# Kernel tuning notes

Measured on AMD Instinct MI355X. Metric: run time of the kernel, lower is better.

Reference implementation:

```python
import jax, jax.numpy as jnp
import numpy as np

# SparseSphereConv (graph_level=6 -> V=40962, kernel_size=9, stride=1, select_index=None)
# Pipeline: neighbor gather -> data-dependent nonzero row selection ->
# per-vertex KxK interpolation matmul -> 1xK conv (linear over C_in,K) -> scatter back.
# With stride=1 / select_index=None the static selection is the identity, so the
# dynamic nonzero selection is equivalent to computing all rows and zeroing the
# rows whose gathered features are entirely zero (selected rows are scattered back,
# unselected rows stay 0 in sparse_reset's zero-initialized output).

BS, C_IN, C_OUT, V, K = 4, 32, 32, 40962, 9

def setup_inputs() -> dict:
    key = jax.random.key(0)
    k1, k2, k3, k4, k5 = jax.random.split(key, 5)
    x = jax.random.normal(k1, (BS, C_IN, V), dtype=jnp.float32)
    index = jax.random.randint(k2, (V, K), 0, V, dtype=jnp.int32)          # neighbor ids per vertex
    itp_mat = jax.random.uniform(k3, (V, K, K), dtype=jnp.float32)         # per-vertex interpolation
    conv_w = jax.random.normal(k4, (C_OUT, C_IN, K), dtype=jnp.float32) * 0.05  # Conv2d(C_in,C_out,(1,K)) weight
    conv_b = jax.random.normal(k5, (C_OUT,), dtype=jnp.float32) * 0.05
    return {"x": x, "index": index, "itp_mat": itp_mat, "conv_w": conv_w, "conv_b": conv_b}

def reference(x, index, itp_mat, conv_w, conv_b):
    # x: [bs, C, V] -> permute(2,0,1) -> gather neighbors -> [V, K, bs, C]
    g = jnp.transpose(x, (2, 0, 1))[index]
    g = jnp.transpose(g, (3, 2, 0, 1))                      # [C, bs, V, K]  (== reshape of [C, bs*V, K])
    # sparse_prepare: keep rows whose min or max over (C, K) is nonzero (detached in torch)
    gd = jax.lax.stop_gradient(g)
    rmin = gd.min(axis=(0, 3))                              # [bs, V]
    rmax = gd.max(axis=(0, 3))                              # [bs, V]
    mask = (rmin != 0) | (rmax != 0)                        # [bs, V]
    # Interploate: [C, S, 1, K] @ [S, K, K] per row -> batched small matmul
    interp = jnp.einsum('cbvk,vkj->cbvj', g, itp_mat)       # [C, bs, V, K]
    # Conv2d with kernel (1, K): contraction over (C_in, K) + bias
    out = jnp.einsum('cbvk,ock->bov', interp, conv_w) + conv_b[None, :, None]  # [bs, C_out, V]
    # sparse_reset: rows not selected stay zero
    return out * mask[:, None, :].astype(out.dtype)
```

## Files before the change

kernel.cpp:

```cpp
#include <hip/hip_runtime.h>
#include <hip/hip_bf16.h>

#define NV 40962
#define NK 9
#define CIN 32
#define COUT 32
#define NBS 4
#define VT 256
#define TP 260
#define NT 2561
#define NV81 (NV * 81)
#define NV9  (NV * 9)

typedef __attribute__((ext_vector_type(8))) short bf16x8;
typedef __attribute__((ext_vector_type(4))) float f32x4;
typedef __attribute__((ext_vector_type(2))) float f32x2;

#define PKFMA_L(A, G, R) asm("v_pk_fma_f32 %0, %1, %2, %0 op_sel:[0,0,0] op_sel_hi:[0,1,1]" : "+v"(A) : "v"(G), "v"(R))
#define PKFMA_H(A, G, R) asm("v_pk_fma_f32 %0, %1, %2, %0 op_sel:[1,0,0] op_sel_hi:[1,1,1]" : "+v"(A) : "v"(G), "v"(R))
#define PKMUL_L(A, G, R) asm("v_pk_mul_f32 %0, %1, %2 op_sel:[0,0] op_sel_hi:[0,1]" : "=v"(A) : "v"(G), "v"(R))
#define PKMUL_H(A, G, R) asm("v_pk_mul_f32 %0, %1, %2 op_sel:[1,0] op_sel_hi:[1,1]" : "=v"(A) : "v"(G), "v"(R))

#define ACC(cc, j) ((j) == 8 ? acc8[cc] : (((j) & 1) ? acc2[cc][(j) >> 1].y \
                                                     : acc2[cc][(j) >> 1].x))

__device__ __forceinline__ unsigned pkbf(float a, float b) {
    union { __hip_bfloat162 h2; unsigned u; } cv;
    cv.h2 = __float22bfloat162_rn(make_float2(a, b));
    return cv.u;
}

__global__ void __launch_bounds__(256) transpose_x_bf16(
    const float* __restrict__ x, unsigned* __restrict__ xtw)
{
    __shared__ unsigned T[16 * TP];
    const int b  = blockIdx.x & 3;
    const int v0 = (blockIdx.x >> 2) * VT;
    const int t  = threadIdx.x;
    const int w  = t >> 6;
    const int L  = t & 63;
    const bool full = (v0 + VT <= NV);

    #pragma unroll
    for (int i = 0; i < 4; ++i) {
        const int q = w + 4 * i;
        const float* rowA = x + (size_t)(b * 32 + 2 * q) * NV;
        const float* rowB = rowA + NV;
        #pragma unroll
        for (int h = 0; h < 2; ++h) {
            const int vl = 128 * h + 2 * L;
            float2 a, c;
            if (full) {
                a = *(const float2*)(rowA + v0 + vl);
                c = *(const float2*)(rowB + v0 + vl);
            } else {
                const int v = v0 + vl;
                a.x = (v     < NV) ? rowA[v]     : 0.0f;
                a.y = (v + 1 < NV) ? rowA[v + 1] : 0.0f;
                c.x = (v     < NV) ? rowB[v]     : 0.0f;
                c.y = (v + 1 < NV) ? rowB[v + 1] : 0.0f;
            }
            uint2 d;
            d.x = pkbf(a.x, c.x);
            d.y = pkbf(a.y, c.y);
            *(uint2*)&T[q * TP + vl] = d;
        }
    }
    __syncthreads();

    #pragma unroll
    for (int i = 0; i < 4; ++i) {
        const int vl = i * 64 + w * 16 + (L >> 2);
        const int u4 = L & 3;
        const int v  = v0 + vl;
        if (v < NV) {
            uint4 d;
            d.x = T[(4 * u4 + 0) * TP + vl];
            d.y = T[(4 * u4 + 1) * TP + vl];
            d.z = T[(4 * u4 + 2) * TP + vl];
            d.w = T[(4 * u4 + 3) * TP + vl];
            *(uint4*)&xtw[(size_t)v * 64 + b * 16 + 4 * u4] = d;
        }
    }
}

__global__ void __launch_bounds__(256) convert_w_bf16(
    const float* __restrict__ w, unsigned short* __restrict__ wbf)
{
    const int i = blockIdx.x * 256 + threadIdx.x;
    if (i < COUT * CIN * NK) {
        const int o = i / 288;
        const int r = i - o * 288;
        const int c = r / 9;
        const int j = r - c * 9;
        unsigned u = __float_as_uint(w[i]);
        wbf[o * 288 + j * 32 + c] =
            (unsigned short)((u + 0x7FFFu + ((u >> 16) & 1u)) >> 16);
    }
}

__global__ void __launch_bounds__(256) sparse_conv_mfma(
    const unsigned short* __restrict__ xt, const int* __restrict__ index,
    const float* __restrict__ itp, const unsigned short* __restrict__ wbf,
    const float* __restrict__ bias, float* __restrict__ out)
{
    __shared__ unsigned short Wlds[9 * 32 * 32];
    __shared__ float itp_s[16 * 108];
    __shared__ int   idx_s[144];

    const int t    = threadIdx.x;
    const int b    = t >> 6;
    const int lane = t & 63;
    const int vloc = lane & 15;
    const int quad = lane >> 4;
    const int tile = blockIdx.x;

    float bs0[4], bs1[4];
    #pragma unroll
    for (int r = 0; r < 4; ++r) {
        bs0[r] = bias[quad * 4 + r];
        bs1[r] = bias[quad * 4 + 16 + r];
    }

    #pragma unroll
    for (int r = 0; r < 5; ++r) {
        const int n = t + r * 256;
        if (n < 1152) {
            const int j  = n >> 7;
            const int o  = (n >> 2) & 31;
            const int cq = n & 3;
            ((uint4*)Wlds)[n] = ((const uint4*)wbf)[o * 36 + j * 4 + cq];
        }
    }
    if (t < 144) {
        const size_t bix = (size_t)tile * 144 + t;
        idx_s[t] = (bix < (size_t)NV9) ? index[bix] : 0;
    }
    {
        float itpv[6];
        const size_t base = (size_t)tile * 1296;
        #pragma unroll
        for (int i = 0; i < 6; ++i) {
            const int o = i * 256 + t;
            itpv[i] = (o < 1296 && base + o < (size_t)NV81) ? itp[base + o]
                                                            : 0.0f;
        }
        #pragma unroll
        for (int i = 0; i < 6; ++i) {
            const int o = i * 256 + t;
            if (o < 1296) {
                const int vl = o / 81;
                const int r2 = o - vl * 81;
                const int kk = r2 / 9;
                const int jj = r2 - kk * 9;
                itp_s[vl * 108 + kk * 12 + jj] = itpv[i];
            }
        }
    }
    __syncthreads();

    int nbr[NK];
    #pragma unroll
    for (int n = 0; n < NK; ++n) nbr[n] = idx_s[vloc * 9 + n];

    const unsigned short* gbase = xt + b * 32 + quad * 8;
    uint2 g0[NK], g1[NK];
    #pragma unroll
    for (int n = 0; n < NK; ++n)
        g0[n] = *(const uint2*)(gbase + (size_t)nbr[n] * 128);
    #pragma unroll
    for (int n = 0; n < NK; ++n)
        g1[n] = *(const uint2*)(gbase + (size_t)nbr[n] * 128 + 4);

    unsigned frag[9][4];
    unsigned nzbits = 0;
    const float* ib = &itp_s[vloc * 108];

    #pragma unroll
    for (int h = 0; h < 2; ++h) {
        f32x2 acc2[4][4];
        float acc8[4];
        #pragma unroll
        for (int n = 0; n < NK; ++n) {
            const uint2 gk = h ? g1[n] : g0[n];
            nzbits |= (gk.x | gk.y) & 0x7FFF7FFFu;
            f32x2 gp01, gp23;
            gp01.x = __uint_as_float(gk.x << 16);
            gp01.y = __uint_as_float(gk.x & 0xFFFF0000u);
            gp23.x = __uint_as_float(gk.y << 16);
            gp23.y = __uint_as_float(gk.y & 0xFFFF0000u);
            const float* ir = ib + n * 12;
            const f32x4 ra = *(const f32x4*)ir;
            const f32x4 rb = *(const f32x4*)(ir + 4);
            const float r8 = ir[8];
            f32x2 rp[4];
            rp[0] = __builtin_shufflevector(ra, ra, 0, 1);
            rp[1] = __builtin_shufflevector(ra, ra, 2, 3);
            rp[2] = __builtin_shufflevector(rb, rb, 0, 1);
            rp[3] = __builtin_shufflevector(rb, rb, 2, 3);
            if (n == 0) {
                #pragma unroll
                for (int jp = 0; jp < 4; ++jp) {
                    PKMUL_L(acc2[0][jp], gp01, rp[jp]);
                    PKMUL_H(acc2[1][jp], gp01, rp[jp]);
                    PKMUL_L(acc2[2][jp], gp23, rp[jp]);
                    PKMUL_H(acc2[3][jp], gp23, rp[jp]);
                }
                acc8[0] = gp01.x * r8; acc8[1] = gp01.y * r8;
                acc8[2] = gp23.x * r8; acc8[3] = gp23.y * r8;
            } else {
                #pragma unroll
                for (int jp = 0; jp < 4; ++jp) {
                    PKFMA_L(acc2[0][jp], gp01, rp[jp]);
                    PKFMA_H(acc2[1][jp], gp01, rp[jp]);
                    PKFMA_L(acc2[2][jp], gp23, rp[jp]);
                    PKFMA_H(acc2[3][jp], gp23, rp[jp]);
                }
                acc8[0] += gp01.x * r8; acc8[1] += gp01.y * r8;
                acc8[2] += gp23.x * r8; acc8[3] += gp23.y * r8;
            }
        }
        #pragma unroll
        for (int ks = 0; ks < 9; ++ks) {
            frag[ks][2 * h]     = pkbf(ACC(0, ks), ACC(1, ks));
            frag[ks][2 * h + 1] = pkbf(ACC(2, ks), ACC(3, ks));
        }
    }

    unsigned nzw = nzbits;
    nzw |= __shfl_xor(nzw, 16);
    nzw |= __shfl_xor(nzw, 32);

    f32x4 c0 = {0.f, 0.f, 0.f, 0.f};
    f32x4 c1 = {0.f, 0.f, 0.f, 0.f};
    #pragma unroll
    for (int ks = 0; ks < 9; ++ks) {
        union { uint4 u; bf16x8 v; } bfr;
        bfr.u.x = frag[ks][0]; bfr.u.y = frag[ks][1];
        bfr.u.z = frag[ks][2]; bfr.u.w = frag[ks][3];
        const bf16x8 wa0 =
            *(const bf16x8*)&Wlds[(ks * 32 + vloc) * 32 + quad * 8];
        const bf16x8 wa1 =
            *(const bf16x8*)&Wlds[(ks * 32 + vloc + 16) * 32 + quad * 8];
        c0 = __builtin_amdgcn_mfma_f32_16x16x32_bf16(wa0, bfr.v, c0, 0, 0, 0);
        c1 = __builtin_amdgcn_mfma_f32_16x16x32_bf16(wa1, bfr.v, c1, 0, 0, 0);
    }

    const int vv = tile * 16 + vloc;
    if (vv < NV) {
        const float m = nzw ? 1.0f : 0.0f;
        float* ob = out + (size_t)b * (COUT * NV) + vv;
        #pragma unroll
        for (int r = 0; r < 4; ++r) {
            ob[(size_t)(quad * 4 + r) * NV]      = (c0[r] + bs0[r]) * m;
            ob[(size_t)(quad * 4 + 16 + r) * NV] = (c1[r] + bs1[r]) * m;
        }
    }
}

extern "C" void kernel_launch(void* const* d_in, const int* in_sizes, int n_in,
                              void* d_out, int out_size, void* d_ws, size_t ws_size,
                              hipStream_t stream)
{
    const float* x     = (const float*)d_in[0];
    const int*   index = (const int*)  d_in[1];
    const float* itp   = (const float*)d_in[2];
    const float* w     = (const float*)d_in[3];
    const float* bias  = (const float*)d_in[4];
    float*       out   = (float*)d_out;

    unsigned short* xt  = (unsigned short*)d_ws;
    unsigned short* wbf = (unsigned short*)((char*)d_ws + (size_t)NV * 256);

    hipLaunchKernelGGL(convert_w_bf16, dim3((COUT * CIN * NK + 255) / 256),
                       dim3(256), 0, stream, w, wbf);
    const int vtiles = (NV + VT - 1) / VT;
    hipLaunchKernelGGL(transpose_x_bf16, dim3(vtiles * NBS), dim3(256), 0,
                       stream, x, (unsigned*)xt);
    hipLaunchKernelGGL(sparse_conv_mfma, dim3(NT), dim3(256), 0,
                       stream, xt, index, itp, wbf, bias, out);
}
```

Before: 128.3 us.

## Remap lanes to batch-by-vertex and interleave bf16 layout for 16-byte gathers

The transposed bf16 buffer is re-laid out so that, for each vertex, the four batches of one 8-channel group sit next to each other. The conv kernel's lane mapping changes so each wave covers 4 vertices by 4 batches instead of 16 vertices of one batch. Each lane now fetches a neighbor's features with one 16-byte load instead of two 8-byte loads, and the lanes serving one vertex together read its full 256-byte row. The aim is fewer, better-coalesced gather transactions. The trade-off is that output stores now cover only 4 consecutive vertices per row segment, which weakens store coalescing.

```diff
diff --git a/kernel.cpp b/kernel.cpp
--- a/kernel.cpp
+++ b/kernel.cpp
@@ -79,7 +79,7 @@
             d.y = T[(4 * u4 + 1) * TP + vl];
             d.z = T[(4 * u4 + 2) * TP + vl];
             d.w = T[(4 * u4 + 3) * TP + vl];
-            *(uint4*)&xtw[(size_t)v * 64 + b * 16 + 4 * u4] = d;
+            *(uint4*)&xtw[(size_t)v * 64 + u4 * 16 + b * 4] = d;
         }
     }
 }
@@ -109,17 +109,20 @@
     __shared__ int   idx_s[144];
 
     const int t    = threadIdx.x;
-    const int b    = t >> 6;
+    const int w    = t >> 6;
     const int lane = t & 63;
-    const int vloc = lane & 15;
-    const int quad = lane >> 4;
+    const int arow = lane & 15;
+    const int coct = lane >> 4;
+    const int b    = (lane >> 2) & 3;
+    const int vv   = lane & 3;
+    const int vl   = w * 4 + vv;
     const int tile = blockIdx.x;
 
     float bs0[4], bs1[4];
     #pragma unroll
     for (int r = 0; r < 4; ++r) {
-        bs0[r] = bias[quad * 4 + r];
-        bs1[r] = bias[quad * 4 + 16 + r];
+        bs0[r] = bias[coct * 4 + r];
+        bs1[r] = bias[coct * 4 + 16 + r];
     }
 
     #pragma unroll
@@ -149,11 +152,11 @@
         for (int i = 0; i < 6; ++i) {
             const int o = i * 256 + t;
             if (o < 1296) {
-                const int vl = o / 81;
-                const int r2 = o - vl * 81;
+                const int vli = o / 81;
+                const int r2 = o - vli * 81;
                 const int kk = r2 / 9;
                 const int jj = r2 - kk * 9;
-                itp_s[vl * 108 + kk * 12 + jj] = itpv[i];
+                itp_s[vli * 108 + kk * 12 + jj] = itpv[i];
             }
         }
     }
@@ -161,20 +164,17 @@
 
     int nbr[NK];
     #pragma unroll
-    for (int n = 0; n < NK; ++n) nbr[n] = idx_s[vloc * 9 + n];
-
-    const unsigned short* gbase = xt + b * 32 + quad * 8;
-    uint2 g0[NK], g1[NK];
+    for (int n = 0; n < NK; ++n) nbr[n] = idx_s[vl * 9 + n];
+
+    const unsigned short* gbase = xt + coct * 32 + b * 8;
+    uint4 g[NK];
     #pragma unroll
     for (int n = 0; n < NK; ++n)
-        g0[n] = *(const uint2*)(gbase + (size_t)nbr[n] * 128);
-    #pragma unroll
-    for (int n = 0; n < NK; ++n)
-        g1[n] = *(const uint2*)(gbase + (size_t)nbr[n] * 128 + 4);
+        g[n] = *(const uint4*)(gbase + (size_t)nbr[n] * 128);
 
     unsigned frag[9][4];
     unsigned nzbits = 0;
-    const float* ib = &itp_s[vloc * 108];
+    const float* ib = &itp_s[vl * 108];
 
     #pragma unroll
     for (int h = 0; h < 2; ++h) {
@@ -182,7 +182,8 @@
         float acc8[4];
         #pragma unroll
         for (int n = 0; n < NK; ++n) {
-            const uint2 gk = h ? g1[n] : g0[n];
+            const uint2 gk = h ? make_uint2(g[n].z, g[n].w)
+                               : make_uint2(g[n].x, g[n].y);
             nzbits |= (gk.x | gk.y) & 0x7FFF7FFFu;
             f32x2 gp01, gp23;
             gp01.x = __uint_as_float(gk.x << 16);
@@ -239,21 +240,21 @@
         bfr.u.x = frag[ks][0]; bfr.u.y = frag[ks][1];
         bfr.u.z = frag[ks][2]; bfr.u.w = frag[ks][3];
         const bf16x8 wa0 =
-            *(const bf16x8*)&Wlds[(ks * 32 + vloc) * 32 + quad * 8];
+            *(const bf16x8*)&Wlds[(ks * 32 + arow) * 32 + coct * 8];
         const bf16x8 wa1 =
-            *(const bf16x8*)&Wlds[(ks * 32 + vloc + 16) * 32 + quad * 8];
+            *(const bf16x8*)&Wlds[(ks * 32 + arow + 16) * 32 + coct * 8];
         c0 = __builtin_amdgcn_mfma_f32_16x16x32_bf16(wa0, bfr.v, c0, 0, 0, 0);
         c1 = __builtin_amdgcn_mfma_f32_16x16x32_bf16(wa1, bfr.v, c1, 0, 0, 0);
     }
 
-    const int vv = tile * 16 + vloc;
-    if (vv < NV) {
+    const int vglob = tile * 16 + vl;
+    if (vglob < NV) {
         const float m = nzw ? 1.0f : 0.0f;
-        float* ob = out + (size_t)b * (COUT * NV) + vv;
+        float* ob = out + (size_t)b * (COUT * NV) + vglob;
         #pragma unroll
         for (int r = 0; r < 4; ++r) {
-            ob[(size_t)(quad * 4 + r) * NV]      = (c0[r] + bs0[r]) * m;
-            ob[(size_t)(quad * 4 + 16 + r) * NV] = (c1[r] + bs1[r]) * m;
+            ob[(size_t)(coct * 4 + r) * NV]      = (c0[r] + bs0[r]) * m;
+            ob[(size_t)(coct * 4 + 16 + r) * NV] = (c1[r] + bs1[r]) * m;
         }
     }
 }
```

Measured after the change: 135.9 us. 5.9% more time.
